# Kernel optimization log

Hardware: AMD Instinct MI355X
Metric: run time of the kernel (lower is better)

## Reference

```python
import jax, jax.numpy as jnp
import numpy as np
from jax import lax

EPS = 1e-6

def _class_wise_pool(x, g):
    # torch ClassWisePool: average groups of g consecutive channels
    b, c, h, w = x.shape
    return x.reshape(b, c // g, g, h, w).mean(axis=2)

def _conv1x1(wgt, bias, t):
    return jnp.einsum('oi,bihw->bohw', wgt, t) + bias[None, :, None, None]

def setup_inputs() -> dict:
    key = jax.random.key(0)
    ks = jax.random.split(key, 13)
    B, H, W = 64, 14, 14
    f = lambda k, s, sc=1.0: jax.random.normal(k, s, dtype=jnp.float32) * sc
    return {
        'r5': f(ks[0], (B, 2048, H, W)),
        'fc0_w': f(ks[1], (512, 2048, 3, 3), 0.01),
        'bn_gamma': 1.0 + 0.1 * f(ks[2], (512,)),
        'bn_beta': 0.1 * f(ks[3], (512,)),
        'bn_mean': 0.1 * f(ks[4], (512,)),
        'bn_var': 0.5 + jax.random.uniform(ks[5], (512,), dtype=jnp.float32),
        'mu0': f(ks[6], (512, 8)),
        'conv4_w': f(ks[7], (2048, 4096), 0.02),
        'conv4_b': jnp.zeros((2048,), jnp.float32),
        'down_w': f(ks[8], (32, 2048), 0.02),
        'down_b': jnp.zeros((32,), jnp.float32),
        'cls_w': f(ks[9], (8, 4096), 0.02),
        'cls_b': jnp.zeros((8,), jnp.float32),
    }

def reference(r5, fc0_w, bn_gamma, bn_beta, bn_mean, bn_var, mu0,
              conv4_w, conv4_b, down_w, down_b, cls_w, cls_b):
    B, _, H, W = r5.shape
    N = H * W
    K = 8  # emotional categories

    # fc0: Conv3x3 -> BN(eval) -> ReLU, 2048 -> 512
    y = lax.conv_general_dilated(r5, fc0_w, (1, 1), ((1, 1), (1, 1)),
                                 dimension_numbers=('NCHW', 'OIHW', 'NCHW'))
    y = (y - bn_mean[:, None, None]) * (bn_gamma / jnp.sqrt(bn_var + 1e-5))[:, None, None] + bn_beta[:, None, None]
    y = jax.nn.relu(y)

    # CAE / EM attention (EMANet-style), stage_num = 3
    x = y.reshape(B, 512, N)
    mu = mu0 / (jnp.linalg.norm(mu0, axis=0, keepdims=True) + EPS)  # [512, K]
    mu = jnp.broadcast_to(mu[None], (B, 512, K))
    z = None
    for _ in range(3):
        z = jax.nn.softmax(jnp.einsum('bcn,bck->bnk', x, mu), axis=-1)  # [B,N,K]
        zn = z / (z.sum(axis=1, keepdims=True) + EPS)
        mu = jnp.einsum('bcn,bnk->bck', x, zn)
        mu = mu / (jnp.linalg.norm(mu, axis=1, keepdims=True) + EPS)
    x_r = jnp.einsum('bck,bnk->bcn', mu, z)
    x2 = jax.nn.relu(x + x_r).reshape(B, 512, H, W)  # GCEM output
    z_t = z.transpose(0, 2, 1).reshape(B, K, H, W)   # attention map

    # class_att = z_t.view(b,8,1,h,w).mean(2) == z_t
    # per-class matmul loop + 8 cats -> single einsum, channel order i-major
    x1 = jnp.einsum('bchw,bkwv->bkchv', x2, z_t).reshape(B, K * 512, H, W)

    dic_global = _conv1x1(conv4_w, conv4_b, x1)             # [B,2048,H,W]
    xb = jnp.concatenate([r5 * dic_global, r5], axis=1)     # [B,4096,H,W]
    xb = _conv1x1(conv4_w, conv4_b, xb)                     # same conv4 reused

    xd = _conv1x1(down_w, down_b, xb)                       # downconv [B,32,H,W]
    xg = _class_wise_pool(xd.mean(axis=(2, 3), keepdims=True), 4).reshape(B, 8)  # GAP + pool
    xc = _class_wise_pool(xd, 4) * xg[:, :, None, None]     # [B,8,H,W]
    xc = _class_wise_pool(xc, 8)                            # [B,1,H,W]

    # 2047 sequential torch.cat == broadcast to 2048 channels
    xcopy = jnp.broadcast_to(xc, (B, 2048, H, W)) * r5
    xcopy = jnp.concatenate([r5, xcopy], axis=1).mean(axis=(2, 3))  # GAP -> [B,4096]
    out2 = xcopy @ cls_w.T + cls_b
    return (xg, out2)
```

## Files before the change

kernel.cpp:

```cpp
#include <hip/hip_runtime.h>
#include <hip/hip_bf16.h>

typedef unsigned short u16;
typedef unsigned int   u32;
typedef __attribute__((ext_vector_type(4))) float f32x4;
typedef __attribute__((ext_vector_type(8))) short s16x8;

__device__ __forceinline__ float b2f(u16 u){ u32 x = ((u32)u) << 16; return __builtin_bit_cast(float, x); }
__device__ __forceinline__ u16 f2b(float f){
  u32 x = __builtin_bit_cast(u32, f);
  u32 r = (x + 0x7FFFu + ((x >> 16) & 1u)) >> 16;
  return (u16)r;
}
__device__ __forceinline__ float inld(const void* p, size_t i, int isbf){
  return isbf ? b2f(((const u16*)p)[i]) : ((const float*)p)[i];
}
__device__ __forceinline__ u16 inld16(const void* p, size_t i, int isbf){
  return isbf ? ((const u16*)p)[i] : f2b(((const float*)p)[i]);
}

__device__ __forceinline__ void async16(const void* g, void* l){
  __builtin_amdgcn_global_load_lds((const __attribute__((address_space(1))) void*)g,
                                   (__attribute__((address_space(3))) void*)l, 16, 0, 0);
}

__global__ __launch_bounds__(256) void detect_kernel(const u32* __restrict__ r5w, int* __restrict__ flag){
  __shared__ int cnt[2];
  int t = threadIdx.x;
  if (t < 2) cnt[t] = 0;
  __syncthreads();
  int inw = 0, nz = 0;
  for (int i = t; i < 16384; i += 256){
    u32 w = r5w[i];
    if (w == 0u) continue;
    u32 e = (w >> 7) & 0xFFu;
    nz++;
    if (e >= 0x58u && e <= 0x98u) inw++;
  }
  atomicAdd(&cnt[0], inw);
  atomicAdd(&cnt[1], nz);
  __syncthreads();
  if (t == 0) flag[0] = (2 * cnt[0] >= cnt[1]) ? 1 : 0;
}

__global__ __launch_bounds__(256) void prep_kernel(
    const void* __restrict__ g, const void* __restrict__ be,
    const void* __restrict__ mn, const void* __restrict__ vr,
    const void* __restrict__ dw, const void* __restrict__ db,
    const void* __restrict__ b4, const int* __restrict__ flag,
    float* __restrict__ scale, float* __restrict__ bias,
    u16* __restrict__ dwp, float* __restrict__ dbp,
    u16* __restrict__ b4c, u16* __restrict__ zrow)
{
  const int isbf = *flag;
  int idx = blockIdx.x * 256 + threadIdx.x;
  if (idx < 512){
    float s = inld(g, idx, isbf) / sqrtf(inld(vr, idx, isbf) + 1e-5f);
    scale[idx] = s;
    bias[idx]  = inld(be, idx, isbf) - inld(mn, idx, isbf) * s;
  }
  if (idx < 128) dbp[idx] = (idx < 32) ? inld(db, idx, isbf) : 0.f;
  if (idx < 2048){
    zrow[idx] = 0;
    b4c[idx] = inld16(b4, idx, isbf);
  }
  if (idx < 128 * 2048){
    int j = idx >> 11;
    dwp[idx] = (j < 32) ? inld16(dw, idx, isbf) : (u16)0;
  }
}

__global__ __launch_bounds__(256) void wt_pack(const void* __restrict__ w, const int* __restrict__ flag,
                                               u16* __restrict__ wt){
  const int isbf = *flag;
  int idx = blockIdx.x * 256 + threadIdx.x;
  if (idx >= 512 * 18432) return;
  int o = idx / 18432;
  int r = idx - o * 18432;
  int tap = r >> 11, i = r & 2047;
  wt[idx] = inld16(w, ((size_t)(o * 2048 + i)) * 9 + tap, isbf);
}

__global__ __launch_bounds__(256) void cvt_w4(const void* __restrict__ w4, const int* __restrict__ flag,
                                              u16* __restrict__ w4c){
  const int isbf = *flag;
  int idx = blockIdx.x * 256 + threadIdx.x;
  if (idx < 2048 * 4096) w4c[idx] = inld16(w4, idx, isbf);
}

__global__ __launch_bounds__(256) void transpose_r5(const void* __restrict__ r5, size_t elem_off,
                                                    const int* __restrict__ flag, u16* __restrict__ r5nk){
  __shared__ u16 tile[64 * 197];
  const int isbf = *flag;
  int blk = blockIdx.x;
  int b = blk >> 5, c0 = (blk & 31) * 64;
  int t = threadIdx.x;
  size_t src = elem_off + ((size_t)b * 2048 + c0) * 196;
  for (int q = t; q < 64 * 196; q += 256){
    int cl = q / 196, hv = q - cl * 196;
    tile[cl * 197 + hv] = inld16(r5, src + q, isbf);
  }
  __syncthreads();
  for (int q = t; q < 64 * 196; q += 256){
    int hv = q >> 6, cl = q & 63;
    r5nk[((size_t)b * 196 + hv) * 2048 + c0 + cl] = tile[cl * 197 + hv];
  }
}

template<int MODE>
__global__ __launch_bounds__(256) void gemm_bt(
    const u16* __restrict__ Aptr, const u16* __restrict__ A2,
    const u16* __restrict__ Bw, void* __restrict__ Cout,
    const float* __restrict__ sc, const float* __restrict__ bi,
    const u16* __restrict__ bias16, const u16* __restrict__ zrow,
    int K, int ldA, int Mrows)
{
  constexpr bool SWAPG = (MODE == 1 || MODE == 2);
  __shared__ u16 As[128 * 32];
  __shared__ u16 Bs[128 * 32];
  const int tid = threadIdx.x;
  const int wv = tid >> 6, ln = tid & 63;
  const int m0 = (SWAPG ? blockIdx.y : blockIdx.x) * 128;
  const int o0 = (SWAPG ? blockIdx.x : blockIdx.y) * 128;

  const int rowA0 = wv * 32 + (ln >> 2);
  const int kofs  = (ln & 3) * 8;
  int mA0 = m0 + rowA0, mA1 = mA0 + 16;
  if (mA0 >= Mrows) mA0 = Mrows - 1;
  if (mA1 >= Mrows) mA1 = Mrows - 1;
  const int oB0 = o0 + rowA0, oB1 = oB0 + 16;

  int h0 = 0, v0 = 0, h1 = 0, v1 = 0;
  if constexpr (MODE == 0){
    int hv0 = mA0 % 196; h0 = hv0 / 14; v0 = hv0 - h0 * 14;
    int hv1 = mA1 % 196; h1 = hv1 / 14; v1 = hv1 - h1 * 14;
  }

  const int wm = (wv >> 1) * 64, wn = (wv & 1) * 64;
  const int fl = ln & 15, fq = ln >> 4;

  f32x4 acc[4][4];
  #pragma unroll
  for (int i = 0; i < 4; i++)
    #pragma unroll
    for (int j = 0; j < 4; j++) acc[i][j] = (f32x4){0.f, 0.f, 0.f, 0.f};

  u16* ldsA0 = &As[wv * 1024];
  u16* ldsA1 = &As[wv * 1024 + 512];
  u16* ldsB0 = &Bs[wv * 1024];
  u16* ldsB1 = &Bs[wv * 1024 + 512];

  for (int k0 = 0; k0 < K; k0 += 32){
    const u16 *ga0, *ga1;
    if constexpr (MODE == 0){
      int tap = k0 >> 11;
      int kin = (k0 & 2047) + kofs;
      int dy = tap / 3 - 1, dx = tap - (tap / 3) * 3 - 1;
      int dlt = dy * 14 + dx;
      bool ok0 = ((unsigned)(h0 + dy) < 14u) && ((unsigned)(v0 + dx) < 14u);
      bool ok1 = ((unsigned)(h1 + dy) < 14u) && ((unsigned)(v1 + dx) < 14u);
      ga0 = ok0 ? Aptr + (size_t)(mA0 + dlt) * 2048 + kin : zrow + kofs;
      ga1 = ok1 ? Aptr + (size_t)(mA1 + dlt) * 2048 + kin : zrow + kofs;
    } else if constexpr (MODE == 2){
      const u16* base = (k0 < 2048) ? Aptr : A2;
      int kin = (k0 & 2047) + kofs;
      ga0 = base + (size_t)mA0 * 2048 + kin;
      ga1 = base + (size_t)mA1 * 2048 + kin;
    } else {
      ga0 = Aptr + (size_t)mA0 * ldA + k0 + kofs;
      ga1 = Aptr + (size_t)mA1 * ldA + k0 + kofs;
    }
    const u16* gb0 = Bw + (size_t)oB0 * K + k0 + kofs;
    const u16* gb1 = Bw + (size_t)oB1 * K + k0 + kofs;

    async16(ga0, ldsA0);
    async16(ga1, ldsA1);
    async16(gb0, ldsB0);
    async16(gb1, ldsB1);
    __syncthreads();

    s16x8 af[4], bfr[4];
    #pragma unroll
    for (int i = 0; i < 4; i++)
      af[i] = *(const s16x8*)&As[(wm + i * 16 + fl) * 32 + fq * 8];
    #pragma unroll
    for (int j = 0; j < 4; j++)
      bfr[j] = *(const s16x8*)&Bs[(wn + j * 16 + fl) * 32 + fq * 8];
    #pragma unroll
    for (int i = 0; i < 4; i++)
      #pragma unroll
      for (int j = 0; j < 4; j++)
        acc[i][j] = __builtin_amdgcn_mfma_f32_16x16x32_bf16(af[i], bfr[j], acc[i][j], 0, 0, 0);
    __syncthreads();
  }

  #pragma unroll
  for (int i = 0; i < 4; i++){
    int mrow = m0 + wm + i * 16 + fq * 4;
    #pragma unroll
    for (int j = 0; j < 4; j++){
      int o = o0 + wn + j * 16 + fl;
      f32x4 a = acc[i][j];
      #pragma unroll
      for (int r = 0; r < 4; r++){
        int n = mrow + r;
        if (n >= Mrows) continue;
        float v = a[r];
        if constexpr (MODE == 0){
          v = fmaxf(v * sc[o] + bi[o], 0.f);
          ((u16*)Cout)[(size_t)n * 512 + o] = f2b(v);
        } else if constexpr (MODE == 1){
          v += b2f(bias16[o]);
          v *= b2f(A2[(size_t)n * 2048 + o]);
          ((u16*)Cout)[(size_t)n * 2048 + o] = f2b(v);
        } else if constexpr (MODE == 2){
          v += b2f(bias16[o]);
          ((u16*)Cout)[(size_t)n * 2048 + o] = f2b(v);
        } else {
          ((float*)Cout)[(size_t)n * 128 + o] = v + bi[o];
        }
      }
    }
  }
}

__global__ __launch_bounds__(512) void em_kernel(
    const u16* __restrict__ x, const void* __restrict__ mu0, const int* __restrict__ flag,
    u16* __restrict__ x2, float* __restrict__ zg)
{
  __shared__ float mu[512][9];
  __shared__ float zz[196][9];
  __shared__ float part[64][8];
  __shared__ float red8[8];
  const int isbf = *flag;
  const int b = blockIdx.x;
  const int t = threadIdx.x;
  const u16* xb = x + (size_t)b * 196 * 512;

  for (int q = t; q < 4096; q += 512) mu[q >> 3][q & 7] = inld(mu0, q, isbf);
  __syncthreads();
  { int k = t & 7, g = t >> 3; float s = 0;
    for (int c = g; c < 512; c += 64){ float m = mu[c][k]; s += m * m; }
    part[g][k] = s; }
  __syncthreads();
  if (t < 8){ float s = 0; for (int g = 0; g < 64; g++) s += part[g][t]; red8[t] = sqrtf(s) + 1e-6f; }
  __syncthreads();
  for (int q = t; q < 4096; q += 512) mu[q >> 3][q & 7] /= red8[q & 7];
  __syncthreads();

  for (int it = 0; it < 3; it++){
    for (int p = t; p < 1568; p += 512){
      int n = p >> 3, k = p & 7;
      const u16* xr = xb + n * 512;
      float s = 0;
      for (int c = 0; c < 512; c += 8){
        uint4 u = *(const uint4*)(xr + c);
        s += b2f((u16)(u.x & 0xffff)) * mu[c][k]     + b2f((u16)(u.x >> 16)) * mu[c + 1][k]
           + b2f((u16)(u.y & 0xffff)) * mu[c + 2][k] + b2f((u16)(u.y >> 16)) * mu[c + 3][k]
           + b2f((u16)(u.z & 0xffff)) * mu[c + 4][k] + b2f((u16)(u.z >> 16)) * mu[c + 5][k]
           + b2f((u16)(u.w & 0xffff)) * mu[c + 6][k] + b2f((u16)(u.w >> 16)) * mu[c + 7][k];
      }
      zz[n][k] = s;
    }
    __syncthreads();
    if (t < 196){
      float mx = zz[t][0];
      #pragma unroll
      for (int k = 1; k < 8; k++) mx = fmaxf(mx, zz[t][k]);
      float e[8], sm = 0;
      #pragma unroll
      for (int k = 0; k < 8; k++){ e[k] = expf(zz[t][k] - mx); sm += e[k]; }
      #pragma unroll
      for (int k = 0; k < 8; k++) zz[t][k] = e[k] / sm;
    }
    __syncthreads();
    { int k = t & 7, g = t >> 3; float s = 0;
      for (int n = g; n < 196; n += 64) s += zz[n][k];
      part[g][k] = s; }
    __syncthreads();
    if (t < 8){ float s = 0; for (int g = 0; g < 64; g++) s += part[g][t]; red8[t] = s + 1e-6f; }
    __syncthreads();
    {
      int c = t;
      float s[8];
      #pragma unroll
      for (int k = 0; k < 8; k++) s[k] = 0.f;
      for (int n = 0; n < 196; n++){
        float xv = b2f(xb[n * 512 + c]);
        #pragma unroll
        for (int k = 0; k < 8; k++) s[k] += xv * zz[n][k];
      }
      __syncthreads();
      #pragma unroll
      for (int k = 0; k < 8; k++) mu[c][k] = s[k] / red8[k];
    }
    __syncthreads();
    { int k = t & 7, g = t >> 3; float s = 0;
      for (int c = g; c < 512; c += 64){ float m = mu[c][k]; s += m * m; }
      part[g][k] = s; }
    __syncthreads();
    if (t < 8){ float s = 0; for (int g = 0; g < 64; g++) s += part[g][t]; red8[t] = sqrtf(s) + 1e-6f; }
    __syncthreads();
    for (int q = t; q < 4096; q += 512) mu[q >> 3][q & 7] /= red8[q & 7];
    __syncthreads();
  }

  for (int p = t; p < 1568; p += 512) zg[b * 1568 + p] = zz[p >> 3][p & 7];
  for (int q = t; q < 196 * 512; q += 512){
    int n = q >> 9, c = q & 511;
    float xr = 0;
    #pragma unroll
    for (int k = 0; k < 8; k++) xr += mu[c][k] * zz[n][k];
    float v = b2f(xb[n * 512 + c]) + xr;
    x2[(size_t)b * 196 * 512 + q] = f2b(fmaxf(v, 0.f));
  }
}

__global__ __launch_bounds__(256) void expand_kernel(
    const u16* __restrict__ x2, const float* __restrict__ zg, u16* __restrict__ x1)
{
  __shared__ u16 xs[14 * 512];
  __shared__ float zb[196 * 8];
  int bh = blockIdx.x;
  int b = bh / 14, h = bh - b * 14;
  int t = threadIdx.x;
  const u16* src = x2 + ((size_t)b * 196 + h * 14) * 512;
  for (int q = t; q < 14 * 512; q += 256) xs[q] = src[q];
  for (int q = t; q < 1568; q += 256) zb[q] = zg[b * 1568 + q];
  __syncthreads();
  size_t outbase = ((size_t)b * 196 + h * 14) * 4096;
  for (int q = t; q < 14 * 4096; q += 256){
    int v = q >> 12, kc = q & 4095;
    int k = kc >> 9, c = kc & 511;
    float s = 0;
    #pragma unroll
    for (int w = 0; w < 14; w++)
      s += b2f(xs[w * 512 + c]) * zb[(w * 14 + v) * 8 + k];
    x1[outbase + q] = f2b(s);
  }
}

__global__ __launch_bounds__(256) void pool_xg(
    const float* __restrict__ xd, const int* __restrict__ flag,
    float* __restrict__ g32, void* __restrict__ outbase, int elem_off)
{
  __shared__ float part[8][32];
  int b = blockIdx.x, t = threadIdx.x;
  int j = t & 31, g = t >> 5;
  float s = 0;
  for (int hv = g; hv < 196; hv += 8)
    s += xd[((size_t)b * 196 + hv) * 128 + j];
  part[g][j] = s;
  __syncthreads();
  if (t < 32){
    float s2 = 0;
    #pragma unroll
    for (int g2 = 0; g2 < 8; g2++) s2 += part[g2][t];
    part[0][t] = s2 * (1.f / 196.f);
  }
  __syncthreads();
  if (t < 8){
    float v = 0.25f * (part[0][4 * t] + part[0][4 * t + 1] + part[0][4 * t + 2] + part[0][4 * t + 3]);
    g32[b * 8 + t] = v;
    int o = elem_off + b * 8 + t;
    if (*flag) ((u16*)outbase)[o] = f2b(v);
    else       ((float*)outbase)[o] = v;
  }
}

__global__ __launch_bounds__(256) void final_kernel(
    const float* __restrict__ xd, const float* __restrict__ g32,
    const u16* __restrict__ r5nk, const void* __restrict__ clsw,
    const void* __restrict__ clsb, const int* __restrict__ flag,
    void* __restrict__ outbase, int elem_off)
{
  __shared__ float xc[196];
  __shared__ float red[8];
  const int isbf = *flag;
  int b = blockIdx.x, t = threadIdx.x;
  if (t < 196){
    float s = 0;
    const float* row = xd + ((size_t)b * 196 + t) * 128;
    #pragma unroll
    for (int j = 0; j < 32; j++) s += row[j] * g32[b * 8 + (j >> 2)];
    xc[t] = s * (1.f / 32.f);
  }
  if (t < 8) red[t] = 0.f;
  __syncthreads();
  float s1[8], s2[8];
  #pragma unroll
  for (int ci = 0; ci < 8; ci++){ s1[ci] = 0.f; s2[ci] = 0.f; }
  for (int hv = 0; hv < 196; hv++){
    const u16* row = r5nk + ((size_t)b * 196 + hv) * 2048;
    float xcv = xc[hv];
    #pragma unroll
    for (int ci = 0; ci < 8; ci++){
      float v = b2f(row[t + ci * 256]);
      s1[ci] += v; s2[ci] += v * xcv;
    }
  }
  float pm[8];
  #pragma unroll
  for (int m = 0; m < 8; m++) pm[m] = 0.f;
  #pragma unroll
  for (int ci = 0; ci < 8; ci++){
    int c = t + ci * 256;
    float a1 = s1[ci] * (1.f / 196.f), a2 = s2[ci] * (1.f / 196.f);
    #pragma unroll
    for (int m = 0; m < 8; m++)
      pm[m] += inld(clsw, m * 4096 + c, isbf) * a1 + inld(clsw, m * 4096 + 2048 + c, isbf) * a2;
  }
  #pragma unroll
  for (int m = 0; m < 8; m++) atomicAdd(&red[m], pm[m]);
  __syncthreads();
  if (t < 8){
    float v = red[t] + inld(clsb, t, isbf);
    int o = elem_off + b * 8 + t;
    if (isbf) ((u16*)outbase)[o] = f2b(v);
    else      ((float*)outbase)[o] = v;
  }
}

extern "C" void kernel_launch(void* const* d_in, const int* in_sizes, int n_in,
                              void* d_out, int out_size, void* d_ws, size_t ws_size,
                              hipStream_t stream)
{
  (void)in_sizes; (void)n_in; (void)out_size;
  const void* r5  = d_in[0];
  const void* fcw = d_in[1];
  const void* bng = d_in[2];
  const void* bnb = d_in[3];
  const void* bnm = d_in[4];
  const void* bnv = d_in[5];
  const void* mu0 = d_in[6];
  const void* w4  = d_in[7];
  const void* b4  = d_in[8];
  const void* dw  = d_in[9];
  const void* db  = d_in[10];
  const void* cw  = d_in[11];
  const void* cb  = d_in[12];

  auto foot = [](int nb)->size_t{
    return 42ull * 1024 * 1024 + (size_t)nb * 3670016ull;
  };
  int NB = 4;
  if (foot(64) <= ws_size) NB = 64;
  else if (foot(32) <= ws_size) NB = 32;
  else if (foot(16) <= ws_size) NB = 16;
  else if (foot(8) <= ws_size) NB = 8;
  const int rowsP = NB * 196;
  const int tiles = (rowsP + 127) / 128;
  const int passes = 64 / NB;

  char* base = (char*)d_ws;
  size_t off = 0;
  auto take = [&](size_t bytes)->char*{
    char* r = base + off;
    off = (off + bytes + 255) & ~(size_t)255;
    return r;
  };

  int*   flag = (int*)  take(256);
  float* scale= (float*)take(512 * 4);
  float* bias = (float*)take(512 * 4);
  float* dbp  = (float*)take(128 * 4);
  u16*   zrow = (u16*)  take(2048 * 2);
  u16*   b4c  = (u16*)  take(2048 * 2);
  float* g32  = (float*)take(64 * 8 * 4);
  u16*   dwp  = (u16*)  take(128 * 2048 * 2);
  float* zg   = (float*)take(64ULL * 1568 * 4);
  u16*   Wt   = (u16*)  take(512ULL * 18432 * 2);
  u16*   w4c  = (u16*)  take(2048ULL * 4096 * 2);
  u16*   r5nk = (u16*)  take((size_t)rowsP * 2048 * 2);
  u16*   regX = (u16*)  take((size_t)rowsP * 4096 * 2);
  u16*   bufC = (u16*)  take((size_t)rowsP * 2048 * 2);
  u16*   x2b  = (u16*)  take((size_t)rowsP * 512 * 2);
  float* xd   = (float*)take((size_t)rowsP * 128 * 4);

  u16* x1  = regX;
  u16* c2  = regX;
  u16* xnk = bufC;
  u16* xbA = bufC;

  detect_kernel<<<1, 256, 0, stream>>>((const u32*)r5, flag);
  prep_kernel<<<1024, 256, 0, stream>>>(bng, bnb, bnm, bnv, dw, db, b4, flag,
                                        scale, bias, dwp, dbp, b4c, zrow);
  wt_pack<<<(512 * 18432 + 255) / 256, 256, 0, stream>>>(fcw, flag, Wt);
  cvt_w4<<<(2048 * 4096) / 256, 256, 0, stream>>>(w4, flag, w4c);

  for (int p = 0; p < passes; p++){
    size_t r5off = (size_t)p * NB * 2048 * 196;
    int oxg = p * NB * 8;
    int oo2 = 512 + p * NB * 8;

    transpose_r5<<<NB * 32, 256, 0, stream>>>(r5, r5off, flag, r5nk);
    gemm_bt<0><<<dim3(tiles, 4), 256, 0, stream>>>(r5nk, nullptr, Wt, xnk, scale, bias, nullptr, zrow, 18432, 2048, rowsP);
    em_kernel<<<NB, 512, 0, stream>>>(xnk, mu0, flag, x2b, zg);
    expand_kernel<<<NB * 14, 256, 0, stream>>>(x2b, zg, x1);
    gemm_bt<1><<<dim3(16, tiles), 256, 0, stream>>>(x1, r5nk, w4c, xbA, nullptr, nullptr, b4c, zrow, 4096, 4096, rowsP);
    gemm_bt<2><<<dim3(16, tiles), 256, 0, stream>>>(xbA, r5nk, w4c, c2, nullptr, nullptr, b4c, zrow, 4096, 2048, rowsP);
    gemm_bt<3><<<dim3(tiles, 1), 256, 0, stream>>>(c2, nullptr, dwp, xd, nullptr, dbp, nullptr, zrow, 2048, 2048, rowsP);
    pool_xg<<<NB, 256, 0, stream>>>(xd, flag, g32, d_out, oxg);
    final_kernel<<<NB, 256, 0, stream>>>(xd, g32, r5nk, cw, cb, flag, d_out, oo2);
  }
}
```

Baseline: 1.836 ms.

## Double GEMM K-tile to 64 with XOR-swizzled LDS layout

Raises the K step of the bf16 MFMA GEMM from 32 to 64, so each thread issues four async 16-byte loads per operand per iteration and the block synchronises half as often per unit of K. The LDS rows are now 64 elements wide, with the 8-element chunk index XOR-swizzled by row to avoid bank conflicts on fragment reads. The aim is to amortise barrier and load-issue overhead over twice the MFMA work. In exchange, LDS use doubles to 32KB per block, which may reduce occupancy, and there is still no double buffering.

```diff
diff --git a/kernel.cpp b/kernel.cpp
--- a/kernel.cpp
+++ b/kernel.cpp
@@ -116,28 +116,35 @@
     int K, int ldA, int Mrows)
 {
   constexpr bool SWAPG = (MODE == 1 || MODE == 2);
-  __shared__ u16 As[128 * 32];
-  __shared__ u16 Bs[128 * 32];
+  __shared__ u16 As[128 * 64];
+  __shared__ u16 Bs[128 * 64];
   const int tid = threadIdx.x;
   const int wv = tid >> 6, ln = tid & 63;
   const int m0 = (SWAPG ? blockIdx.y : blockIdx.x) * 128;
   const int o0 = (SWAPG ? blockIdx.x : blockIdx.y) * 128;
 
-  const int rowA0 = wv * 32 + (ln >> 2);
-  const int kofs  = (ln & 3) * 8;
-  int mA0 = m0 + rowA0, mA1 = mA0 + 16;
-  if (mA0 >= Mrows) mA0 = Mrows - 1;
-  if (mA1 >= Mrows) mA1 = Mrows - 1;
-  const int oB0 = o0 + rowA0, oB1 = oB0 + 16;
-
-  int h0 = 0, v0 = 0, h1 = 0, v1 = 0;
-  if constexpr (MODE == 0){
-    int hv0 = mA0 % 196; h0 = hv0 / 14; v0 = hv0 - h0 * 14;
-    int hv1 = mA1 % 196; h1 = hv1 / 14; v1 = hv1 - h1 * 14;
+  const int sub = ln >> 3;
+  const int kq  = (ln & 7) ^ sub;
+  const int kofs = kq * 8;
+
+  int mA[4];
+  int hA[4], vA[4];
+  int oB[4];
+  #pragma unroll
+  for (int i = 0; i < 4; i++){
+    int r = m0 + wv * 32 + i * 8 + sub;
+    if (r >= Mrows) r = Mrows - 1;
+    mA[i] = r;
+    if constexpr (MODE == 0){
+      int hv = r % 196;
+      hA[i] = hv / 14; vA[i] = hv - hA[i] * 14;
+    }
+    oB[i] = o0 + wv * 32 + i * 8 + sub;
   }
 
   const int wm = (wv >> 1) * 64, wn = (wv & 1) * 64;
   const int fl = ln & 15, fq = ln >> 4;
+  const int fl7 = fl & 7;
 
   f32x4 acc[4][4];
   #pragma unroll
@@ -145,52 +152,49 @@
     #pragma unroll
     for (int j = 0; j < 4; j++) acc[i][j] = (f32x4){0.f, 0.f, 0.f, 0.f};
 
-  u16* ldsA0 = &As[wv * 1024];
-  u16* ldsA1 = &As[wv * 1024 + 512];
-  u16* ldsB0 = &Bs[wv * 1024];
-  u16* ldsB1 = &Bs[wv * 1024 + 512];
-
-  for (int k0 = 0; k0 < K; k0 += 32){
-    const u16 *ga0, *ga1;
-    if constexpr (MODE == 0){
-      int tap = k0 >> 11;
-      int kin = (k0 & 2047) + kofs;
-      int dy = tap / 3 - 1, dx = tap - (tap / 3) * 3 - 1;
-      int dlt = dy * 14 + dx;
-      bool ok0 = ((unsigned)(h0 + dy) < 14u) && ((unsigned)(v0 + dx) < 14u);
-      bool ok1 = ((unsigned)(h1 + dy) < 14u) && ((unsigned)(v1 + dx) < 14u);
-      ga0 = ok0 ? Aptr + (size_t)(mA0 + dlt) * 2048 + kin : zrow + kofs;
-      ga1 = ok1 ? Aptr + (size_t)(mA1 + dlt) * 2048 + kin : zrow + kofs;
-    } else if constexpr (MODE == 2){
-      const u16* base = (k0 < 2048) ? Aptr : A2;
-      int kin = (k0 & 2047) + kofs;
-      ga0 = base + (size_t)mA0 * 2048 + kin;
-      ga1 = base + (size_t)mA1 * 2048 + kin;
-    } else {
-      ga0 = Aptr + (size_t)mA0 * ldA + k0 + kofs;
-      ga1 = Aptr + (size_t)mA1 * ldA + k0 + kofs;
-    }
-    const u16* gb0 = Bw + (size_t)oB0 * K + k0 + kofs;
-    const u16* gb1 = Bw + (size_t)oB1 * K + k0 + kofs;
-
-    async16(ga0, ldsA0);
-    async16(ga1, ldsA1);
-    async16(gb0, ldsB0);
-    async16(gb1, ldsB1);
-    __syncthreads();
-
-    s16x8 af[4], bfr[4];
-    #pragma unroll
-    for (int i = 0; i < 4; i++)
-      af[i] = *(const s16x8*)&As[(wm + i * 16 + fl) * 32 + fq * 8];
-    #pragma unroll
-    for (int j = 0; j < 4; j++)
-      bfr[j] = *(const s16x8*)&Bs[(wn + j * 16 + fl) * 32 + fq * 8];
-    #pragma unroll
-    for (int i = 0; i < 4; i++)
+  for (int k0 = 0; k0 < K; k0 += 64){
+    #pragma unroll
+    for (int i = 0; i < 4; i++){
+      const u16* ga;
+      if constexpr (MODE == 0){
+        int tap = k0 >> 11;
+        int kin = (k0 & 2047) + kofs;
+        int dy = tap / 3 - 1, dx = tap - (tap / 3) * 3 - 1;
+        int dlt = dy * 14 + dx;
+        bool ok = ((unsigned)(hA[i] + dy) < 14u) && ((unsigned)(vA[i] + dx) < 14u);
+        ga = ok ? Aptr + (size_t)(mA[i] + dlt) * 2048 + kin : zrow + kofs;
+      } else if constexpr (MODE == 2){
+        const u16* base = (k0 < 2048) ? Aptr : A2;
+        int kin = (k0 & 2047) + kofs;
+        ga = base + (size_t)mA[i] * 2048 + kin;
+      } else {
+        ga = Aptr + (size_t)mA[i] * ldA + k0 + kofs;
+      }
+      async16(ga, &As[wv * 2048 + i * 512]);
+    }
+    #pragma unroll
+    for (int i = 0; i < 4; i++){
+      const u16* gb = Bw + (size_t)oB[i] * K + k0 + kofs;
+      async16(gb, &Bs[wv * 2048 + i * 512]);
+    }
+    __syncthreads();
+
+    #pragma unroll
+    for (int s = 0; s < 2; s++){
+      const int pos = ((fq + 4 * s) ^ fl7) * 8;
+      s16x8 af[4], bfr[4];
+      #pragma unroll
+      for (int i = 0; i < 4; i++)
+        af[i] = *(const s16x8*)&As[(wm + i * 16 + fl) * 64 + pos];
       #pragma unroll
       for (int j = 0; j < 4; j++)
-        acc[i][j] = __builtin_amdgcn_mfma_f32_16x16x32_bf16(af[i], bfr[j], acc[i][j], 0, 0, 0);
+        bfr[j] = *(const s16x8*)&Bs[(wn + j * 16 + fl) * 64 + pos];
+      #pragma unroll
+      for (int i = 0; i < 4; i++)
+        #pragma unroll
+        for (int j = 0; j < 4; j++)
+          acc[i][j] = __builtin_amdgcn_mfma_f32_16x16x32_bf16(af[i], bfr[j], acc[i][j], 0, 0, 0);
+    }
     __syncthreads();
   }
 
```

Result: faster. 1.687 ms (-8.1%).
